# Performance work log

Hardware: AMD Instinct MI355X
Metric: run time of the kernel (lower is better)

## Reference

```python
import jax, jax.numpy as jnp
import numpy as np

N = 8000        # nodes
E = 64000       # directed edges (before self-loops)
F_IN = 3201     # node_dim=1 + encoding_dim(128)*25
N_TRAIN = 4000


def setup_inputs() -> dict:
    key = jax.random.key(0)
    k = jax.random.split(key, 4)
    d = {
        'x': jax.random.normal(k[0], (N, F_IN), dtype=jnp.float32),
        'edge_index': jax.random.randint(k[1], (2, E), 0, N),
        'y': jax.random.uniform(k[2], (N,), dtype=jnp.float32),
        'train_idx': jax.random.randint(k[3], (N_TRAIN,), 0, N),
    }
    cnt = [0]
    def w(shape, fan_in):
        cnt[0] += 1
        kk = jax.random.fold_in(jax.random.key(1), cnt[0])
        return (jax.random.normal(kk, shape, dtype=jnp.float32) / np.float32(np.sqrt(fan_in)))
    ones = lambda n: jnp.ones((n,), jnp.float32)
    zeros = lambda n: jnp.zeros((n,), jnp.float32)
    d['bn0_g'] = ones(F_IN); d['bn0_b'] = zeros(F_IN)
    d['W1l'] = w((F_IN, 1024), F_IN); d['W1r'] = w((F_IN, 1024), F_IN)
    d['a1'] = w((2, 512), 512); d['b1'] = zeros(1024)
    d['bn1_g'] = ones(1024); d['bn1_b'] = zeros(1024)
    d['W2l'] = w((1024, 512), 1024); d['W2r'] = w((1024, 512), 1024)
    d['a2'] = w((1, 512), 512); d['b2'] = zeros(512)
    d['bn2_g'] = ones(512); d['bn2_b'] = zeros(512)
    d['W3l'] = w((512, 512), 512); d['W3r'] = w((512, 512), 512)
    d['a3'] = w((1, 512), 512); d['b3'] = zeros(512)
    d['bn3_g'] = ones(512); d['bn3_b'] = zeros(512)
    d['W4l'] = w((512, 512), 512); d['W4r'] = w((512, 512), 512)
    d['a4'] = w((1, 512), 512); d['b4'] = zeros(512)
    d['Wh'] = w((512, 1), 512); d['bh'] = zeros(1)
    return d


def _batchnorm(h, g, b, eps=1e-5):
    # training-mode batch statistics over the node dim
    m = h.mean(axis=0)
    v = h.var(axis=0)
    return (h - m) * jax.lax.rsqrt(v + jnp.float32(eps)) * g + b


def _gatv2(h, src, dst, Wl, Wr, att, bias, n):
    # GATv2Conv with concat heads, softmax over incoming edges, aggr='mean'
    H, C = att.shape
    xl = (h @ Wl).reshape(n, H, C)   # source transform
    xr = (h @ Wr).reshape(n, H, C)   # target transform
    z = jax.nn.leaky_relu(xl[src] + xr[dst], negative_slope=0.2)  # [E,H,C]
    e = jnp.einsum('ehc,hc->eh', z, att)                          # [E,H]
    emax = jax.ops.segment_max(e, dst, num_segments=n)            # segment softmax
    ex = jnp.exp(e - emax[dst])
    denom = jax.ops.segment_sum(ex, dst, num_segments=n)
    alpha = ex / denom[dst]
    agg = jax.ops.segment_sum(alpha[:, :, None] * xl[src], dst, num_segments=n)
    deg = jax.ops.segment_sum(jnp.ones(src.shape[0], h.dtype), dst, num_segments=n)
    return (agg / deg[:, None, None]).reshape(n, H * C) + bias


def reference(x, edge_index, y, train_idx, bn0_g, bn0_b, W1l, W1r, a1, b1,
              bn1_g, bn1_b, W2l, W2r, a2, b2, bn2_g, bn2_b, W3l, W3r, a3, b3,
              bn3_g, bn3_b, W4l, W4r, a4, b4, Wh, bh):
    n = x.shape[0]
    loops = jnp.arange(n, dtype=edge_index.dtype)  # PyG add_self_loops=True
    src = jnp.concatenate([edge_index[0], loops])
    dst = jnp.concatenate([edge_index[1], loops])
    h = _batchnorm(x, bn0_g, bn0_b)
    h = _gatv2(h, src, dst, W1l, W1r, a1, b1, n)          # -> [N,1024]
    h = jax.nn.relu(_batchnorm(h, bn1_g, bn1_b))
    h = _gatv2(h, src, dst, W2l, W2r, a2, b2, n)          # -> [N,512]
    h = jax.nn.relu(_batchnorm(h, bn2_g, bn2_b))
    h = _gatv2(h, src, dst, W3l, W3r, a3, b3, n)
    h = jax.nn.relu(_batchnorm(h, bn3_g, bn3_b))
    h = jax.nn.relu(_gatv2(h, src, dst, W4l, W4r, a4, b4, n))
    pred = jax.nn.sigmoid(h @ Wh + bh)[:, 0]              # [N]
    return pred[train_idx], y[train_idx]
```

## Files before the change

### kernel.cpp

```cpp
#include <hip/hip_runtime.h>
#include <math.h>

typedef __bf16 bf16x8 __attribute__((ext_vector_type(8)));
typedef float f32x16 __attribute__((ext_vector_type(16)));
typedef unsigned short ushort8 __attribute__((ext_vector_type(8)));

__device__ __forceinline__ float bf2f(unsigned short u) {
  union { unsigned int i; float f; } c; c.i = ((unsigned int)u) << 16; return c.f;
}
__device__ __forceinline__ unsigned short f2bf(float f) {
  union { float f; unsigned int i; } c; c.f = f;
  unsigned int r = (c.i + 0x7fffu + ((c.i >> 16) & 1u)) >> 16;
  return (unsigned short)r;
}

__global__ void zero_k(float* __restrict__ statz, int nz, int* __restrict__ deg, int n) {
  int i = blockIdx.x * blockDim.x + threadIdx.x;
  if (i < nz) statz[i] = 0.f;
  if (i < n) deg[i] = 1;
}

__global__ void deg_count_k(const int* __restrict__ dst, int* __restrict__ deg, int e) {
  int i = blockIdx.x * blockDim.x + threadIdx.x;
  if (i < e) atomicAdd(&deg[dst[i]], 1);
}

__global__ void scan_k(const int* __restrict__ deg, int* __restrict__ offsets,
                       int* __restrict__ cursor, int n) {
  __shared__ int sums[1024];
  int tid = threadIdx.x;
  int chunk = (n + 1023) >> 10;
  int base = tid * chunk;
  int s = 0;
  for (int i = 0; i < chunk; ++i) {
    int j = base + i;
    if (j < n) s += deg[j];
  }
  sums[tid] = s;
  __syncthreads();
  for (int off = 1; off < 1024; off <<= 1) {
    int v = (tid >= off) ? sums[tid - off] : 0;
    __syncthreads();
    sums[tid] += v;
    __syncthreads();
  }
  int run = sums[tid] - s;
  for (int i = 0; i < chunk; ++i) {
    int j = base + i;
    if (j < n) {
      offsets[j] = run;
      cursor[j] = run;
      run += deg[j];
    }
  }
  if (tid == 1023) offsets[n] = sums[1023];
}

__global__ void csr_fill_k(const int* __restrict__ src, const int* __restrict__ dst,
                           int* __restrict__ cursor, int* __restrict__ csr_src,
                           int e, int n) {
  int i = blockIdx.x * blockDim.x + threadIdx.x;
  if (i >= e + n) return;
  int s, d;
  if (i < e) { s = src[i]; d = dst[i]; }
  else       { s = i - e;  d = s; }
  int pos = atomicAdd(&cursor[d], 1);
  csr_src[pos] = s;
}

__global__ __launch_bounds__(256)
void stats_convert_k(const float* __restrict__ x, unsigned short* __restrict__ Abf,
                     float* __restrict__ s1, float* __restrict__ s2,
                     int M, int K, int Kp) {
  int c = blockIdx.x * 256 + threadIdx.x;
  if (c >= Kp) return;
  int rows = (M + gridDim.y - 1) / gridDim.y;
  int r0 = blockIdx.y * rows;
  int r1 = min(M, r0 + rows);
  if (c >= K) {
    for (int r = r0; r < r1; ++r) Abf[(size_t)r * Kp + c] = 0;
    return;
  }
  float a = 0.f, b = 0.f;
  int r = r0;
  for (; r + 4 <= r1; r += 4) {
    float v0 = x[(size_t)(r + 0) * K + c];
    float v1 = x[(size_t)(r + 1) * K + c];
    float v2 = x[(size_t)(r + 2) * K + c];
    float v3 = x[(size_t)(r + 3) * K + c];
    a += v0 + v1 + v2 + v3;
    b += v0 * v0 + v1 * v1 + v2 * v2 + v3 * v3;
    Abf[(size_t)(r + 0) * Kp + c] = f2bf(v0);
    Abf[(size_t)(r + 1) * Kp + c] = f2bf(v1);
    Abf[(size_t)(r + 2) * Kp + c] = f2bf(v2);
    Abf[(size_t)(r + 3) * Kp + c] = f2bf(v3);
  }
  for (; r < r1; ++r) {
    float v = x[(size_t)r * K + c];
    a += v; b += v * v;
    Abf[(size_t)r * Kp + c] = f2bf(v);
  }
  atomicAdd(&s1[c], a);
  atomicAdd(&s2[c], b);
}

__global__ __launch_bounds__(256)
void col_stats_bf_k(const unsigned short* __restrict__ h, int M, int D,
                    float* __restrict__ s1, float* __restrict__ s2) {
  int c = blockIdx.x * 256 + threadIdx.x;
  if (c >= D) return;
  int rows = (M + gridDim.y - 1) / gridDim.y;
  int r0 = blockIdx.y * rows;
  int r1 = min(M, r0 + rows);
  float a = 0.f, b = 0.f;
  int r = r0;
  for (; r + 4 <= r1; r += 4) {
    float v0 = bf2f(h[(size_t)(r + 0) * D + c]);
    float v1 = bf2f(h[(size_t)(r + 1) * D + c]);
    float v2 = bf2f(h[(size_t)(r + 2) * D + c]);
    float v3 = bf2f(h[(size_t)(r + 3) * D + c]);
    a += v0 + v1 + v2 + v3;
    b += v0 * v0 + v1 * v1 + v2 * v2 + v3 * v3;
  }
  for (; r < r1; ++r) {
    float v = bf2f(h[(size_t)r * D + c]);
    a += v; b += v * v;
  }
  atomicAdd(&s1[c], a);
  atomicAdd(&s2[c], b);
}

__global__ __launch_bounds__(256)
void bn_apply8_k(const unsigned short* __restrict__ h,
                 const float* __restrict__ s1, const float* __restrict__ s2,
                 const float* __restrict__ g, const float* __restrict__ b,
                 unsigned short* __restrict__ outb,
                 size_t total, int D, float invM) {
  size_t i = ((size_t)blockIdx.x * 256 + threadIdx.x) * 8;
  if (i >= total) return;
  ushort8 u = *(const ushort8*)(h + i);
  int c = (int)(i % (size_t)D);
  ushort8 o;
#pragma unroll
  for (int j = 0; j < 8; ++j) {
    float m = s1[c + j] * invM;
    float var = fmaxf(s2[c + j] * invM - m * m, 0.f);
    float a = rsqrtf(var + 1e-5f) * g[c + j];
    float cc = b[c + j] - m * a;
    float v = bf2f(u[j]) * a + cc;
    o[j] = f2bf(fmaxf(v, 0.f));
  }
  *(ushort8*)(outb + i) = o;
}

__global__ __launch_bounds__(256)
void wconv_pair_k(const float* __restrict__ Wl, const float* __restrict__ Wr,
                  unsigned short* __restrict__ WT, int K, int N, int Kp,
                  const float* __restrict__ s1, const float* __restrict__ s2,
                  const float* __restrict__ gg, const float* __restrict__ bb,
                  float* __restrict__ bias, float invM) {
  const float* W = blockIdx.z ? Wr : Wl;
  unsigned short* WTo = WT + (size_t)blockIdx.z * N * Kp;
  __shared__ float t[32][33];
  int n0 = blockIdx.x * 32, k0 = blockIdx.y * 32;
  int tx = threadIdx.x & 31, ty = threadIdx.x >> 5;
  float bsum = 0.f;
#pragma unroll
  for (int i = 0; i < 32; i += 8) {
    int k = k0 + ty + i, nn = n0 + tx;
    float v = (k < K && nn < N) ? W[(size_t)k * N + nn] : 0.f;
    t[ty + i][tx] = v;
    if (s1 && k < K) {
      float m = s1[k] * invM;
      float var = fmaxf(s2[k] * invM - m * m, 0.f);
      float a = rsqrtf(var + 1e-5f) * gg[k];
      float c = bb[k] - m * a;
      bsum += c * v;
    }
  }
  if (s1) atomicAdd(&bias[blockIdx.z * N + n0 + tx], bsum);
  float ascale = 1.f;
  if (s1) {
    int k = k0 + tx;
    if (k < K) {
      float m = s1[k] * invM;
      float var = fmaxf(s2[k] * invM - m * m, 0.f);
      ascale = rsqrtf(var + 1e-5f) * gg[k];
    }
  }
  __syncthreads();
#pragma unroll
  for (int i = 0; i < 32; i += 8) {
    int nn = n0 + ty + i, k = k0 + tx;
    if (nn < N && k < Kp) {
      float v = t[tx][ty + i] * ascale;
      WTo[(size_t)nn * Kp + k] = f2bf(v);
    }
  }
}

__global__ __launch_bounds__(256)
void gemm_bf16_k(const unsigned short* __restrict__ A,
                 const unsigned short* __restrict__ Bt,
                 unsigned short* __restrict__ outL, unsigned short* __restrict__ outR,
                 const float* __restrict__ bias, int M, int Nh, int K) {
  __shared__ unsigned short sA[128 * 64];
  __shared__ unsigned short sB[128 * 64];
  const int tid = threadIdx.x;
  const int wave = tid >> 6, lane = tid & 63;
  const int wm = wave >> 1, wn = wave & 1;
  const int l32 = lane & 31, lh = lane >> 5;
  const int row0 = blockIdx.y * 128, col0 = blockIdx.x * 128;

  f32x16 acc[2][2] = {};

  for (int kt = 0; kt < K; kt += 64) {
#pragma unroll
    for (int i = 0; i < 4; ++i) {
      int s = i * 256 + tid;
      int r = s >> 3;
      int g = (s & 7) ^ (r & 7);
      int ra = row0 + r;
      ra = ra < M ? ra : M - 1;
      const unsigned short* ga = A + (size_t)ra * K + (kt + g * 8);
      __builtin_amdgcn_global_load_lds(
          (const __attribute__((address_space(1))) void*)ga,
          (__attribute__((address_space(3))) void*)&sA[s * 8], 16, 0, 0);
      const unsigned short* gb = Bt + (size_t)(col0 + r) * K + (kt + g * 8);
      __builtin_amdgcn_global_load_lds(
          (const __attribute__((address_space(1))) void*)gb,
          (__attribute__((address_space(3))) void*)&sB[s * 8], 16, 0, 0);
    }
    __syncthreads();
#pragma unroll
    for (int s = 0; s < 4; ++s) {
      int g = s * 2 + lh;
      bf16x8 af[2], bfr[2];
#pragma unroll
      for (int t = 0; t < 2; ++t) {
        int r = wm * 64 + t * 32 + l32;
        af[t] = *(const bf16x8*)&sA[(r * 8 + (g ^ (r & 7))) * 8];
        int rb = wn * 64 + t * 32 + l32;
        bfr[t] = *(const bf16x8*)&sB[(rb * 8 + (g ^ (rb & 7))) * 8];
      }
#pragma unroll
      for (int mt = 0; mt < 2; ++mt)
#pragma unroll
        for (int nt = 0; nt < 2; ++nt)
          acc[mt][nt] = __builtin_amdgcn_mfma_f32_32x32x16_bf16(af[mt], bfr[nt], acc[mt][nt], 0, 0, 0);
    }
    __syncthreads();
  }
#pragma unroll
  for (int mt = 0; mt < 2; ++mt) {
#pragma unroll
    for (int nt = 0; nt < 2; ++nt) {
      int col = col0 + wn * 64 + nt * 32 + l32;
      float bv = bias ? bias[col] : 0.f;
      unsigned short* base;
      int cc;
      if (col < Nh) { base = outL; cc = col; }
      else          { base = outR; cc = col - Nh; }
      int rb0 = row0 + wm * 64 + mt * 32 + 4 * lh;
#pragma unroll
      for (int r = 0; r < 16; ++r) {
        int rr = rb0 + (r & 3) + 8 * (r >> 2);
        if (rr < M) base[(size_t)rr * Nh + cc] = f2bf(acc[mt][nt][r] + bv);
      }
    }
  }
}

template <int H>
__global__ __launch_bounds__(256)
void gat_edge_k(const unsigned short* __restrict__ xl, const unsigned short* __restrict__ xr,
                const float* __restrict__ att, const float* __restrict__ bias,
                const int* __restrict__ csr, const int* __restrict__ offsets,
                unsigned short* __restrict__ out, int n, int relu) {
  int gw = (blockIdx.x * 256 + threadIdx.x) >> 6;
  int lane = threadIdx.x & 63;
  if (gw >= n * H) return;
  int node, head;
  if (H == 1) { node = gw; head = 0; }
  else        { node = gw >> 1; head = gw & 1; }
  const int W = H * 512;
  const size_t rowoff = (size_t)node * W + head * 512;
  const size_t choff = (size_t)head * 512 + (size_t)(lane * 8);

  float xrv[8], atv[8];
  {
    ushort8 u = *(const ushort8*)(xr + rowoff + lane * 8);
    const float* ap = att + head * 512 + lane * 8;
#pragma unroll
    for (int j = 0; j < 8; ++j) { xrv[j] = bf2f(u[j]); atv[j] = ap[j]; }
  }
  int p0 = offsets[node], p1 = offsets[node + 1];
  ushort8 u0 = *(const ushort8*)(xl + (size_t)csr[p0] * W + choff);
  ushort8 u1 = u0, u2 = u0;
  if (p0 + 1 < p1) u1 = *(const ushort8*)(xl + (size_t)csr[p0 + 1] * W + choff);
  if (p0 + 2 < p1) u2 = *(const ushort8*)(xl + (size_t)csr[p0 + 2] * W + choff);

  float m = -1e30f, l = 0.f;
  float acc[8];
#pragma unroll
  for (int j = 0; j < 8; ++j) acc[j] = 0.f;
  for (int p = p0; p < p1; ++p) {
    ushort8 u = u0;
    u0 = u1; u1 = u2;
    if (p + 3 < p1) u2 = *(const ushort8*)(xl + (size_t)csr[p + 3] * W + choff);
    float lv[8];
    float e = 0.f;
#pragma unroll
    for (int j = 0; j < 8; ++j) {
      lv[j] = bf2f(u[j]);
      float z = lv[j] + xrv[j];
      z = fmaxf(z, 0.f) + 0.2f * fminf(z, 0.f);
      e = fmaf(z, atv[j], e);
    }
#pragma unroll
    for (int off = 32; off > 0; off >>= 1) e += __shfl_xor(e, off, 64);
    float mn = fmaxf(m, e);
    float corr = __expf(m - mn);
    float w = __expf(e - mn);
    l = l * corr + w;
#pragma unroll
    for (int j = 0; j < 8; ++j) acc[j] = acc[j] * corr + w * lv[j];
    m = mn;
  }
  float inv = 1.f / (l * (float)(p1 - p0));
  const float* bp = bias + head * 512 + lane * 8;
  ushort8 o;
#pragma unroll
  for (int j = 0; j < 8; ++j) {
    float v = acc[j] * inv + bp[j];
    if (relu) v = fmaxf(v, 0.f);
    o[j] = f2bf(v);
  }
  *(ushort8*)(out + rowoff + lane * 8) = o;
}

__global__ __launch_bounds__(256)
void head_gather_k(const unsigned short* __restrict__ h, const float* __restrict__ Wh,
                   const float* __restrict__ bh, const float* __restrict__ y,
                   const int* __restrict__ tidx, float* __restrict__ out, int nt) {
  int gw = (blockIdx.x * 256 + threadIdx.x) >> 6;
  int lane = threadIdx.x & 63;
  if (gw >= nt) return;
  int j = tidx[gw];
  ushort8 u = *(const ushort8*)(h + (size_t)j * 512 + lane * 8);
  const float* wp = Wh + lane * 8;
  float s = 0.f;
#pragma unroll
  for (int q = 0; q < 8; ++q) s = fmaf(bf2f(u[q]), wp[q], s);
#pragma unroll
  for (int off = 32; off > 0; off >>= 1) s += __shfl_xor(s, off, 64);
  if (lane == 0) {
    out[gw] = 1.f / (1.f + __expf(-(s + bh[0])));
    out[nt + gw] = y[j];
  }
}

extern "C" void kernel_launch(void* const* d_in, const int* in_sizes, int n_in,
                              void* d_out, int out_size, void* d_ws, size_t ws_size,
                              hipStream_t stream) {
  const float* x     = (const float*)d_in[0];
  const int*   ei    = (const int*)d_in[1];
  const float* y     = (const float*)d_in[2];
  const int*   tidx  = (const int*)d_in[3];
  const float* bn0_g = (const float*)d_in[4];
  const float* bn0_b = (const float*)d_in[5];
  const float* W1l   = (const float*)d_in[6];
  const float* W1r   = (const float*)d_in[7];
  const float* a1    = (const float*)d_in[8];
  const float* b1    = (const float*)d_in[9];
  const float* bn1_g = (const float*)d_in[10];
  const float* bn1_b = (const float*)d_in[11];
  const float* W2l   = (const float*)d_in[12];
  const float* W2r   = (const float*)d_in[13];
  const float* a2    = (const float*)d_in[14];
  const float* b2    = (const float*)d_in[15];
  const float* bn2_g = (const float*)d_in[16];
  const float* bn2_b = (const float*)d_in[17];
  const float* W3l   = (const float*)d_in[18];
  const float* W3r   = (const float*)d_in[19];
  const float* a3    = (const float*)d_in[20];
  const float* b3    = (const float*)d_in[21];
  const float* bn3_g = (const float*)d_in[22];
  const float* bn3_b = (const float*)d_in[23];
  const float* W4l   = (const float*)d_in[24];
  const float* W4r   = (const float*)d_in[25];
  const float* a4    = (const float*)d_in[26];
  const float* b4    = (const float*)d_in[27];
  const float* Wh    = (const float*)d_in[28];
  const float* bh    = (const float*)d_in[29];
  float* out = (float*)d_out;

  const int n   = in_sizes[2];
  const int E   = in_sizes[1] / 2;
  const int FIN = in_sizes[4];
  const int NT  = in_sizes[3];
  const int ET  = E + n;
  const int KP1 = 3264;

  unsigned short* us = (unsigned short*)d_ws;
  const size_t ABF_SZ = (size_t)n * KP1;
  unsigned short* Abf = us;
  unsigned short* hb  = us + ABF_SZ;
  unsigned short* xlb = hb + (size_t)n * 1024;
  unsigned short* xrb = xlb + (size_t)n * 1024;
  float* fp = (float*)(xrb + (size_t)n * 1024);
  float* s1_0  = fp;           fp += 3328;
  float* s2_0  = fp;           fp += 3328;
  float* s1_1  = fp;           fp += 1024;
  float* s2_1  = fp;           fp += 1024;
  float* s1_2  = fp;           fp += 1024;
  float* s2_2  = fp;           fp += 1024;
  float* s1_3  = fp;           fp += 1024;
  float* s2_3  = fp;           fp += 1024;
  float* biasb = fp;           fp += 2048;
  const int kZeroCount = 14848;
  int* deg     = (int*)fp;
  int* offsets = deg + n;
  int* cursor  = offsets + n + 1;
  int* csr     = cursor + n;
  unsigned short* W1T = hb;
  unsigned short* WT  = Abf + (size_t)n * 1024;

  zero_k<<<(kZeroCount + 255) / 256, 256, 0, stream>>>(s1_0, kZeroCount, deg, n);
  deg_count_k<<<(E + 255) / 256, 256, 0, stream>>>(ei + E, deg, E);
  scan_k<<<1, 1024, 0, stream>>>(deg, offsets, cursor, n);
  csr_fill_k<<<(ET + 255) / 256, 256, 0, stream>>>(ei, ei + E, cursor, csr, E, n);

  float invM = 1.f / (float)n;

  {
    dim3 g((KP1 + 255) / 256, 200);
    stats_convert_k<<<g, 256, 0, stream>>>(x, Abf, s1_0, s2_0, n, FIN, KP1);
  }

  {
    dim3 gw1(1024 / 32, KP1 / 32, 2);
    wconv_pair_k<<<gw1, 256, 0, stream>>>(W1l, W1r, W1T, FIN, 1024, KP1,
                                          s1_0, s2_0, bn0_g, bn0_b, biasb, invM);
    dim3 g(1024 / 128, (n + 127) / 128);
    gemm_bf16_k<<<g, 256, 0, stream>>>(Abf, W1T, xlb, xlb, biasb, n, 1024, KP1);
    gemm_bf16_k<<<g, 256, 0, stream>>>(Abf, W1T + (size_t)1024 * KP1, xrb, xrb,
                                       biasb + 1024, n, 1024, KP1);
  }
  gat_edge_k<2><<<(n * 2 + 3) / 4, 256, 0, stream>>>(xlb, xrb, a1, b1, csr, offsets, hb, n, 0);
  {
    dim3 g(1024 / 256, 160);
    col_stats_bf_k<<<g, 256, 0, stream>>>(hb, n, 1024, s1_1, s2_1);
    bn_apply8_k<<<(int)(((size_t)n * 1024 / 8 + 255) / 256), 256, 0, stream>>>(
        hb, s1_1, s2_1, bn1_g, bn1_b, Abf, (size_t)n * 1024, 1024, invM);
  }

  {
    dim3 gw2(512 / 32, 1024 / 32, 2);
    wconv_pair_k<<<gw2, 256, 0, stream>>>(W2l, W2r, WT, 1024, 512, 1024,
                                          nullptr, nullptr, nullptr, nullptr, nullptr, 0.f);
    dim3 g(1024 / 128, (n + 127) / 128);
    gemm_bf16_k<<<g, 256, 0, stream>>>(Abf, WT, xlb, xrb, nullptr, n, 512, 1024);
  }
  gat_edge_k<1><<<(n + 3) / 4, 256, 0, stream>>>(xlb, xrb, a2, b2, csr, offsets, hb, n, 0);
  {
    dim3 g(512 / 256, 160);
    col_stats_bf_k<<<g, 256, 0, stream>>>(hb, n, 512, s1_2, s2_2);
    bn_apply8_k<<<(int)(((size_t)n * 512 / 8 + 255) / 256), 256, 0, stream>>>(
        hb, s1_2, s2_2, bn2_g, bn2_b, Abf, (size_t)n * 512, 512, invM);
  }

  {
    dim3 gw3(512 / 32, 512 / 32, 2);
    wconv_pair_k<<<gw3, 256, 0, stream>>>(W3l, W3r, WT, 512, 512, 512,
                                          nullptr, nullptr, nullptr, nullptr, nullptr, 0.f);
    dim3 g(1024 / 128, (n + 127) / 128);
    gemm_bf16_k<<<g, 256, 0, stream>>>(Abf, WT, xlb, xrb, nullptr, n, 512, 512);
  }
  gat_edge_k<1><<<(n + 3) / 4, 256, 0, stream>>>(xlb, xrb, a3, b3, csr, offsets, hb, n, 0);
  {
    dim3 g(512 / 256, 160);
    col_stats_bf_k<<<g, 256, 0, stream>>>(hb, n, 512, s1_3, s2_3);
    bn_apply8_k<<<(int)(((size_t)n * 512 / 8 + 255) / 256), 256, 0, stream>>>(
        hb, s1_3, s2_3, bn3_g, bn3_b, Abf, (size_t)n * 512, 512, invM);
  }

  {
    dim3 gw4(512 / 32, 512 / 32, 2);
    wconv_pair_k<<<gw4, 256, 0, stream>>>(W4l, W4r, WT, 512, 512, 512,
                                          nullptr, nullptr, nullptr, nullptr, nullptr, 0.f);
    dim3 g(1024 / 128, (n + 127) / 128);
    gemm_bf16_k<<<g, 256, 0, stream>>>(Abf, WT, xlb, xrb, nullptr, n, 512, 512);
  }
  gat_edge_k<1><<<(n + 3) / 4, 256, 0, stream>>>(xlb, xrb, a4, b4, csr, offsets, hb, n, 1);

  head_gather_k<<<(NT + 3) / 4, 256, 0, stream>>>(hb, Wh, bh, y, tidx, out, NT);
}
```

Before: 828.6 us.

## Replace atomic BN stat reductions with partial buffers and a coefficient kernel

Column-stat kernels now write per-row-block partial sums to scratch buffers instead of atomically adding into shared accumulators. A new coef_k reduces these partials once and precomputes the BN scale and shift per column. bn_apply and the weight conversion then read these coefficients instead of recomputing mean, variance and rsqrt per element. The bias fold of the first BN into the layer-1 weights moves into a separate bias_fold_k kernel. This removes atomic contention and redundant per-element math, at the cost of extra launches and scratch memory reused from activation buffers.

```diff
diff --git a/kernel.cpp b/kernel.cpp
--- a/kernel.cpp
+++ b/kernel.cpp
@@ -70,7 +70,7 @@
 
 __global__ __launch_bounds__(256)
 void stats_convert_k(const float* __restrict__ x, unsigned short* __restrict__ Abf,
-                     float* __restrict__ s1, float* __restrict__ s2,
+                     float* __restrict__ P1, float* __restrict__ P2,
                      int M, int K, int Kp) {
   int c = blockIdx.x * 256 + threadIdx.x;
   if (c >= Kp) return;
@@ -100,13 +100,13 @@
     a += v; b += v * v;
     Abf[(size_t)r * Kp + c] = f2bf(v);
   }
-  atomicAdd(&s1[c], a);
-  atomicAdd(&s2[c], b);
+  P1[(size_t)blockIdx.y * Kp + c] = a;
+  P2[(size_t)blockIdx.y * Kp + c] = b;
 }
 
 __global__ __launch_bounds__(256)
 void col_stats_bf_k(const unsigned short* __restrict__ h, int M, int D,
-                    float* __restrict__ s1, float* __restrict__ s2) {
+                    float* __restrict__ P1, float* __restrict__ P2) {
   int c = blockIdx.x * 256 + threadIdx.x;
   if (c >= D) return;
   int rows = (M + gridDim.y - 1) / gridDim.y;
@@ -126,16 +126,46 @@
     float v = bf2f(h[(size_t)r * D + c]);
     a += v; b += v * v;
   }
-  atomicAdd(&s1[c], a);
-  atomicAdd(&s2[c], b);
+  P1[(size_t)blockIdx.y * D + c] = a;
+  P2[(size_t)blockIdx.y * D + c] = b;
+}
+
+__global__ __launch_bounds__(256)
+void coef_k(const float* __restrict__ P1, const float* __restrict__ P2,
+            const float* __restrict__ g, const float* __restrict__ b,
+            float* __restrict__ outA, float* __restrict__ outC,
+            int K, int Kp, int ny, float invM) {
+  int cc = threadIdx.x & 63;
+  int c = blockIdx.x * 64 + cc;
+  int yl = threadIdx.x >> 6;
+  __shared__ float red[2][4][64];
+  float s1 = 0.f, s2 = 0.f;
+  if (c < Kp) {
+#pragma unroll 4
+    for (int y = yl; y < ny; y += 4) {
+      s1 += P1[(size_t)y * Kp + c];
+      s2 += P2[(size_t)y * Kp + c];
+    }
+  }
+  red[0][yl][cc] = s1;
+  red[1][yl][cc] = s2;
+  __syncthreads();
+  if (yl == 0 && c < Kp) {
+    s1 = red[0][0][cc] + red[0][1][cc] + red[0][2][cc] + red[0][3][cc];
+    s2 = red[1][0][cc] + red[1][1][cc] + red[1][2][cc] + red[1][3][cc];
+    if (c >= K) { outA[c] = 0.f; outC[c] = 0.f; return; }
+    float m = s1 * invM;
+    float var = fmaxf(s2 * invM - m * m, 0.f);
+    float a = rsqrtf(var + 1e-5f) * g[c];
+    outA[c] = a;
+    outC[c] = b[c] - m * a;
+  }
 }
 
 __global__ __launch_bounds__(256)
 void bn_apply8_k(const unsigned short* __restrict__ h,
-                 const float* __restrict__ s1, const float* __restrict__ s2,
-                 const float* __restrict__ g, const float* __restrict__ b,
-                 unsigned short* __restrict__ outb,
-                 size_t total, int D, float invM) {
+                 const float* __restrict__ aC, const float* __restrict__ cC,
+                 unsigned short* __restrict__ outb, size_t total, int D) {
   size_t i = ((size_t)blockIdx.x * 256 + threadIdx.x) * 8;
   if (i >= total) return;
   ushort8 u = *(const ushort8*)(h + i);
@@ -143,11 +173,7 @@
   ushort8 o;
 #pragma unroll
   for (int j = 0; j < 8; ++j) {
-    float m = s1[c + j] * invM;
-    float var = fmaxf(s2[c + j] * invM - m * m, 0.f);
-    float a = rsqrtf(var + 1e-5f) * g[c + j];
-    float cc = b[c + j] - m * a;
-    float v = bf2f(u[j]) * a + cc;
+    float v = bf2f(u[j]) * aC[c + j] + cC[c + j];
     o[j] = f2bf(fmaxf(v, 0.f));
   }
   *(ushort8*)(outb + i) = o;
@@ -156,47 +182,58 @@
 __global__ __launch_bounds__(256)
 void wconv_pair_k(const float* __restrict__ Wl, const float* __restrict__ Wr,
                   unsigned short* __restrict__ WT, int K, int N, int Kp,
-                  const float* __restrict__ s1, const float* __restrict__ s2,
-                  const float* __restrict__ gg, const float* __restrict__ bb,
-                  float* __restrict__ bias, float invM) {
+                  const float* __restrict__ coefA) {
   const float* W = blockIdx.z ? Wr : Wl;
   unsigned short* WTo = WT + (size_t)blockIdx.z * N * Kp;
   __shared__ float t[32][33];
   int n0 = blockIdx.x * 32, k0 = blockIdx.y * 32;
   int tx = threadIdx.x & 31, ty = threadIdx.x >> 5;
-  float bsum = 0.f;
 #pragma unroll
   for (int i = 0; i < 32; i += 8) {
     int k = k0 + ty + i, nn = n0 + tx;
     float v = (k < K && nn < N) ? W[(size_t)k * N + nn] : 0.f;
     t[ty + i][tx] = v;
-    if (s1 && k < K) {
-      float m = s1[k] * invM;
-      float var = fmaxf(s2[k] * invM - m * m, 0.f);
-      float a = rsqrtf(var + 1e-5f) * gg[k];
-      float c = bb[k] - m * a;
-      bsum += c * v;
-    }
-  }
-  if (s1) atomicAdd(&bias[blockIdx.z * N + n0 + tx], bsum);
+  }
   float ascale = 1.f;
-  if (s1) {
+  if (coefA) {
     int k = k0 + tx;
-    if (k < K) {
-      float m = s1[k] * invM;
-      float var = fmaxf(s2[k] * invM - m * m, 0.f);
-      ascale = rsqrtf(var + 1e-5f) * gg[k];
-    }
+    ascale = (k < Kp) ? coefA[k] : 0.f;
   }
   __syncthreads();
 #pragma unroll
   for (int i = 0; i < 32; i += 8) {
     int nn = n0 + ty + i, k = k0 + tx;
     if (nn < N && k < Kp) {
-      float v = t[tx][ty + i] * ascale;
-      WTo[(size_t)nn * Kp + k] = f2bf(v);
-    }
-  }
+      WTo[(size_t)nn * Kp + k] = f2bf(t[tx][ty + i] * ascale);
+    }
+  }
+}
+
+__global__ __launch_bounds__(256)
+void bias_fold_k(const float* __restrict__ Wl, const float* __restrict__ Wr,
+                 const float* __restrict__ coefC, float* __restrict__ bias,
+                 int K, int N, int KCH) {
+  int col = blockIdx.x * 256 + threadIdx.x;
+  if (col >= 2 * N) return;
+  const float* W = (col >= N) ? Wr : Wl;
+  int nn = (col >= N) ? col - N : col;
+  int k0 = blockIdx.y * KCH;
+  int k1 = min(K, k0 + KCH);
+  float s = 0.f;
+  int k = k0;
+#pragma unroll 8
+  for (; k + 8 <= k1; k += 8) {
+    s = fmaf(coefC[k + 0], W[(size_t)(k + 0) * N + nn], s);
+    s = fmaf(coefC[k + 1], W[(size_t)(k + 1) * N + nn], s);
+    s = fmaf(coefC[k + 2], W[(size_t)(k + 2) * N + nn], s);
+    s = fmaf(coefC[k + 3], W[(size_t)(k + 3) * N + nn], s);
+    s = fmaf(coefC[k + 4], W[(size_t)(k + 4) * N + nn], s);
+    s = fmaf(coefC[k + 5], W[(size_t)(k + 5) * N + nn], s);
+    s = fmaf(coefC[k + 6], W[(size_t)(k + 6) * N + nn], s);
+    s = fmaf(coefC[k + 7], W[(size_t)(k + 7) * N + nn], s);
+  }
+  for (; k < k1; ++k) s = fmaf(coefC[k], W[(size_t)k * N + nn], s);
+  atomicAdd(&bias[col], s);
 }
 
 __global__ __launch_bounds__(256)
@@ -339,8 +376,7 @@
   *(ushort8*)(out + rowoff + lane * 8) = o;
 }
 
-__global__ __launch_bounds__(256)
-void head_gather_k(const unsigned short* __restrict__ h, const float* __restrict__ Wh,
+__global__ void head_gather_k(const unsigned short* __restrict__ h, const float* __restrict__ Wh,
                    const float* __restrict__ bh, const float* __restrict__ y,
                    const int* __restrict__ tidx, float* __restrict__ out, int nt) {
   int gw = (blockIdx.x * 256 + threadIdx.x) >> 6;
@@ -401,6 +437,8 @@
   const int NT  = in_sizes[3];
   const int ET  = E + n;
   const int KP1 = 3264;
+  const int NY0 = 200;
+  const int NYS = 160;
 
   unsigned short* us = (unsigned short*)d_ws;
   const size_t ABF_SZ = (size_t)n * KP1;
@@ -409,24 +447,25 @@
   unsigned short* xlb = hb + (size_t)n * 1024;
   unsigned short* xrb = xlb + (size_t)n * 1024;
   float* fp = (float*)(xrb + (size_t)n * 1024);
-  float* s1_0  = fp;           fp += 3328;
-  float* s2_0  = fp;           fp += 3328;
-  float* s1_1  = fp;           fp += 1024;
-  float* s2_1  = fp;           fp += 1024;
-  float* s1_2  = fp;           fp += 1024;
-  float* s2_2  = fp;           fp += 1024;
-  float* s1_3  = fp;           fp += 1024;
-  float* s2_3  = fp;           fp += 1024;
   float* biasb = fp;           fp += 2048;
-  const int kZeroCount = 14848;
+  float* coefA = fp;           fp += 3328;
+  float* coefC = fp;           fp += 3328;
+  float* aC    = fp;           fp += 1024;
+  float* cC    = fp;           fp += 1024;
   int* deg     = (int*)fp;
   int* offsets = deg + n;
   int* cursor  = offsets + n + 1;
   int* csr     = cursor + n;
   unsigned short* W1T = hb;
   unsigned short* WT  = Abf + (size_t)n * 1024;
-
-  zero_k<<<(kZeroCount + 255) / 256, 256, 0, stream>>>(s1_0, kZeroCount, deg, n);
+  float* P0a = (float*)hb;
+  float* P0b = P0a + (size_t)NY0 * KP1;
+  float* Psa = (float*)(Abf + (size_t)n * 1024 + 8ull * 1024 * 1024);
+  float* Psb = Psa + (size_t)NYS * 1024;
+
+  const int kZeroCount = 2048;
+  int zmax = n > kZeroCount ? n : kZeroCount;
+  zero_k<<<(zmax + 255) / 256, 256, 0, stream>>>(biasb, kZeroCount, deg, n);
   deg_count_k<<<(E + 255) / 256, 256, 0, stream>>>(ei + E, deg, E);
   scan_k<<<1, 1024, 0, stream>>>(deg, offsets, cursor, n);
   csr_fill_k<<<(ET + 255) / 256, 256, 0, stream>>>(ei, ei + E, cursor, csr, E, n);
@@ -434,14 +473,17 @@
   float invM = 1.f / (float)n;
 
   {
-    dim3 g((KP1 + 255) / 256, 200);
-    stats_convert_k<<<g, 256, 0, stream>>>(x, Abf, s1_0, s2_0, n, FIN, KP1);
+    dim3 g((KP1 + 255) / 256, NY0);
+    stats_convert_k<<<g, 256, 0, stream>>>(x, Abf, P0a, P0b, n, FIN, KP1);
+    coef_k<<<(KP1 + 63) / 64, 256, 0, stream>>>(P0a, P0b, bn0_g, bn0_b,
+                                                coefA, coefC, FIN, KP1, NY0, invM);
   }
 
   {
     dim3 gw1(1024 / 32, KP1 / 32, 2);
-    wconv_pair_k<<<gw1, 256, 0, stream>>>(W1l, W1r, W1T, FIN, 1024, KP1,
-                                          s1_0, s2_0, bn0_g, bn0_b, biasb, invM);
+    wconv_pair_k<<<gw1, 256, 0, stream>>>(W1l, W1r, W1T, FIN, 1024, KP1, coefA);
+    dim3 gb(8, (FIN + 127) / 128);
+    bias_fold_k<<<gb, 256, 0, stream>>>(W1l, W1r, coefC, biasb, FIN, 1024, 128);
     dim3 g(1024 / 128, (n + 127) / 128);
     gemm_bf16_k<<<g, 256, 0, stream>>>(Abf, W1T, xlb, xlb, biasb, n, 1024, KP1);
     gemm_bf16_k<<<g, 256, 0, stream>>>(Abf, W1T + (size_t)1024 * KP1, xrb, xrb,
@@ -449,46 +491,46 @@
   }
   gat_edge_k<2><<<(n * 2 + 3) / 4, 256, 0, stream>>>(xlb, xrb, a1, b1, csr, offsets, hb, n, 0);
   {
-    dim3 g(1024 / 256, 160);
-    col_stats_bf_k<<<g, 256, 0, stream>>>(hb, n, 1024, s1_1, s2_1);
+    dim3 g(1024 / 256, NYS);
+    col_stats_bf_k<<<g, 256, 0, stream>>>(hb, n, 1024, Psa, Psb);
+    coef_k<<<1024 / 64, 256, 0, stream>>>(Psa, Psb, bn1_g, bn1_b, aC, cC, 1024, 1024, NYS, invM);
     bn_apply8_k<<<(int)(((size_t)n * 1024 / 8 + 255) / 256), 256, 0, stream>>>(
-        hb, s1_1, s2_1, bn1_g, bn1_b, Abf, (size_t)n * 1024, 1024, invM);
+        hb, aC, cC, Abf, (size_t)n * 1024, 1024);
   }
 
   {
     dim3 gw2(512 / 32, 1024 / 32, 2);
-    wconv_pair_k<<<gw2, 256, 0, stream>>>(W2l, W2r, WT, 1024, 512, 1024,
-                                          nullptr, nullptr, nullptr, nullptr, nullptr, 0.f);
+    wconv_pair_k<<<gw2, 256, 0, stream>>>(W2l, W2r, WT, 1024, 512, 1024, nullptr);
     dim3 g(1024 / 128, (n + 127) / 128);
     gemm_bf16_k<<<g, 256, 0, stream>>>(Abf, WT, xlb, xrb, nullptr, n, 512, 1024);
   }
   gat_edge_k<1><<<(n + 3) / 4, 256, 0, stream>>>(xlb, xrb, a2, b2, csr, offsets, hb, n, 0);
   {
-    dim3 g(512 / 256, 160);
-    col_stats_bf_k<<<g, 256, 0, stream>>>(hb, n, 512, s1_2, s2_2);
+    dim3 g(512 / 256, NYS);
+    col_stats_bf_k<<<g, 256, 0, stream>>>(hb, n, 512, Psa, Psb);
+    coef_k<<<512 / 64, 256, 0, stream>>>(Psa, Psb, bn2_g, bn2_b, aC, cC, 512, 512, NYS, invM);
     bn_apply8_k<<<(int)(((size_t)n * 512 / 8 + 255) / 256), 256, 0, stream>>>(
-        hb, s1_2, s2_2, bn2_g, bn2_b, Abf, (size_t)n * 512, 512, invM);
+        hb, aC, cC, Abf, (size_t)n * 512, 512);
   }
 
   {
     dim3 gw3(512 / 32, 512 / 32, 2);
-    wconv_pair_k<<<gw3, 256, 0, stream>>>(W3l, W3r, WT, 512, 512, 512,
-                                          nullptr, nullptr, nullptr, nullptr, nullptr, 0.f);
+    wconv_pair_k<<<gw3, 256, 0, stream>>>(W3l, W3r, WT, 512, 512, 512, nullptr);
     dim3 g(1024 / 128, (n + 127) / 128);
     gemm_bf16_k<<<g, 256, 0, stream>>>(Abf, WT, xlb, xrb, nullptr, n, 512, 512);
   }
   gat_edge_k<1><<<(n + 3) / 4, 256, 0, stream>>>(xlb, xrb, a3, b3, csr, offsets, hb, n, 0);
   {
-    dim3 g(512 / 256, 160);
-    col_stats_bf_k<<<g, 256, 0, stream>>>(hb, n, 512, s1_3, s2_3);
+    dim3 g(512 / 256, NYS);
+    col_stats_bf_k<<<g, 256, 0, stream>>>(hb, n, 512, Psa, Psb);
+    coef_k<<<512 / 64, 256, 0, stream>>>(Psa, Psb, bn3_g, bn3_b, aC, cC, 512, 512, NYS, invM);
     bn_apply8_k<<<(int)(((size_t)n * 512 / 8 + 255) / 256), 256, 0, stream>>>(
-        hb, s1_3, s2_3, bn3_g, bn3_b, Abf, (size_t)n * 512, 512, invM);
+        hb, aC, cC, Abf, (size_t)n * 512, 512);
   }
 
   {
     dim3 gw4(512 / 32, 512 / 32, 2);
-    wconv_pair_k<<<gw4, 256, 0, stream>>>(W4l, W4r, WT, 512, 512, 512,
-                                          nullptr, nullptr, nullptr, nullptr, nullptr, 0.f);
+    wconv_pair_k<<<gw4, 256, 0, stream>>>(W4l, W4r, WT, 512, 512, 512, nullptr);
     dim3 g(1024 / 128, (n + 127) / 128);
     gemm_bf16_k<<<g, 256, 0, stream>>>(Abf, WT, xlb, xrb, nullptr, n, 512, 512);
   }
```

After: 753.3 us. 1.1x faster.
